# Optimization experiments

Measured on AMD Instinct MI355X. Metric: run time of the kernel, lower is better.

## Reference

```python
import jax, jax.numpy as jnp
import numpy as np

NUM_HEADS = 16
HEIGHT = 32
WIDTH = 32
FEATURES_DIM = HEIGHT * WIDTH  # 1024
EMBED_DIM = 1024


def setup_inputs() -> dict:
    key = jax.random.key(0)
    ks = jax.random.split(key, 9)
    s_in = 1.0 / np.sqrt(FEATURES_DIM)
    s_e = 1.0 / np.sqrt(EMBED_DIM)
    return {
        "x": jax.random.normal(ks[0], (16, 512, HEIGHT, WIDTH), dtype=jnp.float32),
        "Wq": jax.random.uniform(ks[1], (EMBED_DIM, FEATURES_DIM), jnp.float32, -s_in, s_in),
        "bq": jax.random.uniform(ks[2], (EMBED_DIM,), jnp.float32, -s_in, s_in),
        "Wk": jax.random.uniform(ks[3], (EMBED_DIM, FEATURES_DIM), jnp.float32, -s_in, s_in),
        "bk": jax.random.uniform(ks[4], (EMBED_DIM,), jnp.float32, -s_in, s_in),
        "Wv": jax.random.uniform(ks[5], (EMBED_DIM, FEATURES_DIM), jnp.float32, -s_in, s_in),
        "bv": jax.random.uniform(ks[6], (EMBED_DIM,), jnp.float32, -s_in, s_in),
        "Wo": jax.random.uniform(ks[7], (FEATURES_DIM, EMBED_DIM), jnp.float32, -s_e, s_e),
        "bo": jax.random.uniform(ks[8], (FEATURES_DIM,), jnp.float32, -s_e, s_e),
    }


def reference(x, Wq, bq, Wk, bk, Wv, bv, Wo, bo):
    B, C, H, W = x.shape
    nh = NUM_HEADS
    hd = EMBED_DIM // nh
    xf = x.reshape(B, C, H * W)  # [B, C, F] - channel tokens
    q = xf @ Wq.T + bq  # [B, C, E]
    k = xf @ Wk.T + bk
    v = xf @ Wv.T + bv
    q = q.reshape(B, C, nh, hd).transpose(0, 2, 1, 3)  # [B, nh, C, hd]
    k = k.reshape(B, C, nh, hd).transpose(0, 2, 1, 3)
    v = v.reshape(B, C, nh, hd).transpose(0, 2, 1, 3)
    scores = jnp.einsum("bhcd,bhkd->bhck", q, k) / jnp.sqrt(jnp.float32(hd))
    attn = jax.nn.softmax(scores, axis=-1)
    out = jnp.einsum("bhck,bhkd->bhcd", attn, v)  # [B, nh, C, hd]
    out = out.transpose(0, 2, 1, 3).reshape(B, C, EMBED_DIM)
    out = out @ Wo.T + bo  # [B, C, F]
    return out.reshape(B, C, H, W)
```

## Files before the change

### kernel.cpp

```cpp
#include <hip/hip_runtime.h>


typedef unsigned short u16;
typedef __attribute__((ext_vector_type(8))) short short8;
typedef __attribute__((ext_vector_type(4))) float f32x4;
typedef __attribute__((ext_vector_type(4))) unsigned short u16x4;

#define MFMA16(a, b, c) __builtin_amdgcn_mfma_f32_16x16x32_bf16(a, b, c, 0, 0, 0)

__device__ __forceinline__ u16 f2bf(float x) {
  unsigned u = __float_as_uint(x);
  u += 0x7FFFu + ((u >> 16) & 1u);
  return (u16)(u >> 16);
}

__device__ __forceinline__ void async16(const void* g, void* l) {
  __builtin_amdgcn_global_load_lds(
      (__attribute__((address_space(1))) unsigned int*)(g),
      (__attribute__((address_space(3))) unsigned int*)(l), 16, 0, 0);
}

__global__ __launch_bounds__(256) void cvt_all(
    const float* __restrict__ x, const float* __restrict__ wq,
    const float* __restrict__ wk, const float* __restrict__ wv,
    const float* __restrict__ wo, u16* __restrict__ dst) {
  int g = blockIdx.x * 256 + threadIdx.x;
  const float* s;
  int off;
  if (g < 2097152) {
    s = x; off = g;
  } else {
    int r = g - 2097152;
    int w = r >> 18;
    off = r & 262143;
    s = (w == 0) ? wq : (w == 1) ? wk : (w == 2) ? wv : wo;
  }
  f32x4 v = ((const f32x4*)s)[off];
  u16x4 o;
#pragma unroll
  for (int j = 0; j < 4; ++j) o[j] = f2bf(v[j]);
  ((u16x4*)dst)[g] = o;
}

__device__ __forceinline__ void gemm16(const u16* __restrict__ A,
                                       const u16* __restrict__ W,
                                       int m0, int n0, u16* lds,
                                       f32x4 acc[4][4]) {
  const int t = threadIdx.x;
  const int wave = t >> 6, lane = t & 63, lr = lane & 15, lg = lane >> 4;
  const int wr = wave >> 2, wn = wave & 3;
  const int srow = t >> 3;
  const int scol = ((t & 7) ^ ((t >> 3) & 7)) << 3;
  const u16* gA = A + (size_t)(m0 + srow) * 1024 + scol;
  const u16* gB = W + (size_t)(n0 + srow) * 1024 + scol;
  u16* stA = lds + wave * 512;
  u16* stB = lds + 8192 + wave * 512;
  const int aoff = (wr * 64 + lr) * 64;
  const int boff = 8192 + (wn * 64 + lr) * 64;
  const int sw0 = (lg ^ (lr & 7)) << 3;
  const int sw1 = ((4 ^ lg) ^ (lr & 7)) << 3;

#define STAGEA(buf, k0)                                     \
  {                                                         \
    async16(gA + (k0), stA + (buf) * 24576);                \
    async16(gA + 65536 + (k0), stA + (buf) * 24576 + 4096); \
  }
#define STAGEB1(buf, k0) async16(gB + (k0), stB + (buf) * 24576);
#define STAGEB3(buf, k0)                                       \
  {                                                            \
    async16(gB + 65536 + (k0), stB + (buf) * 24576 + 4096);    \
    async16(gB + 131072 + (k0), stB + (buf) * 24576 + 8192);   \
    async16(gB + 196608 + (k0), stB + (buf) * 24576 + 12288);  \
  }

  STAGEA(0, 0); STAGEB1(0, 0); STAGEB3(0, 0);
  STAGEA(1, 64); STAGEB1(1, 64); STAGEB3(1, 64);
  asm volatile("s_waitcnt vmcnt(6)" ::: "memory");
  __builtin_amdgcn_s_barrier();

#pragma unroll
  for (int tt = 0; tt < 16; ++tt) {
    const u16* bufp = lds + (tt % 3) * 24576;
    const int nb = (tt + 2) % 3, kn = (tt + 2) * 64;
    short8 av[4], bv[4];
#pragma unroll
    for (int m = 0; m < 4; ++m)
      av[m] = *(const short8*)(bufp + aoff + m * 1024 + sw0);
#pragma unroll
    for (int n = 0; n < 4; ++n)
      bv[n] = *(const short8*)(bufp + boff + n * 1024 + sw0);
    if (tt < 14) { STAGEA(nb, kn); STAGEB1(nb, kn); }
    __builtin_amdgcn_s_barrier();
    asm volatile("s_waitcnt lgkmcnt(0)" ::: "memory");
    __builtin_amdgcn_sched_barrier(0);
    __builtin_amdgcn_s_setprio(1);
#pragma unroll
    for (int m = 0; m < 4; ++m)
#pragma unroll
      for (int n = 0; n < 4; ++n)
        acc[m][n] = MFMA16(av[m], bv[n], acc[m][n]);
    __builtin_amdgcn_s_setprio(0);
    __builtin_amdgcn_s_barrier();
#pragma unroll
    for (int m = 0; m < 4; ++m)
      av[m] = *(const short8*)(bufp + aoff + m * 1024 + sw1);
#pragma unroll
    for (int n = 0; n < 4; ++n)
      bv[n] = *(const short8*)(bufp + boff + n * 1024 + sw1);
    if (tt < 14) STAGEB3(nb, kn);
    __builtin_amdgcn_s_barrier();
    asm volatile("s_waitcnt lgkmcnt(0)" ::: "memory");
    __builtin_amdgcn_sched_barrier(0);
    __builtin_amdgcn_s_setprio(1);
#pragma unroll
    for (int m = 0; m < 4; ++m)
#pragma unroll
      for (int n = 0; n < 4; ++n)
        acc[m][n] = MFMA16(av[m], bv[n], acc[m][n]);
    __builtin_amdgcn_s_setprio(0);
    if (tt < 14) {
      asm volatile("s_waitcnt vmcnt(6)" ::: "memory");
    } else {
      asm volatile("s_waitcnt vmcnt(0)" ::: "memory");
    }
    __builtin_amdgcn_s_barrier();
  }
#undef STAGEA
#undef STAGEB1
#undef STAGEB3
}

__global__ __launch_bounds__(512, 2) void gemm_qkv(
    const u16* __restrict__ xb, const u16* __restrict__ wq,
    const u16* __restrict__ wk, const u16* __restrict__ wv,
    const float* __restrict__ bq, const float* __restrict__ bk,
    const float* __restrict__ bv, u16* __restrict__ qo, u16* __restrict__ ko,
    u16* __restrict__ vo) {
  __shared__ u16 lds[73728];
  const int id = blockIdx.x;
  const int lid = (id & 7) * 96 + (id >> 3);
  const int z = lid >> 8;
  const int rem = lid & 255;
  const int m0 = (rem >> 2) * 128, n0 = (rem & 3) * 256;
  const u16* W = (z == 0) ? wq : (z == 1) ? wk : wv;
  const float* bias = (z == 0) ? bq : (z == 1) ? bk : bv;
  u16* outp = (z == 0) ? qo : (z == 1) ? ko : vo;
  f32x4 acc[4][4];
#pragma unroll
  for (int i = 0; i < 4; ++i)
#pragma unroll
    for (int j = 0; j < 4; ++j) acc[i][j] = (f32x4){0.f, 0.f, 0.f, 0.f};
  gemm16(xb, W, m0, n0, lds, acc);

  const int t = threadIdx.x;
  const int wave = t >> 6, lane = t & 63, lr = lane & 15, lg = lane >> 4;
  const int wr = wave >> 2, wn = wave & 3;
  float bb[4];
#pragma unroll
  for (int nf = 0; nf < 4; ++nf) bb[nf] = bias[n0 + wn * 64 + nf * 16 + lr];
#pragma unroll
  for (int mf = 0; mf < 4; ++mf)
#pragma unroll
    for (int nf = 0; nf < 4; ++nf)
#pragma unroll
      for (int r = 0; r < 4; ++r) {
        int m = m0 + wr * 64 + mf * 16 + lg * 4 + r;
        int n = n0 + wn * 64 + nf * 16 + lr;
        float val = acc[mf][nf][r] + bb[nf];
        int b_ = m >> 9, c = m & 511, h = n >> 6, dd = n & 63;
        int idx = (z == 2) ? ((((b_ << 4) + h) << 15) + (dd << 9) + c)
                           : ((((b_ << 4) + h) << 15) + (c << 6) + dd);
        outp[idx] = f2bf(val);
      }
}

__global__ __launch_bounds__(512, 2) void gemm_oproj(const u16* __restrict__ ab,
                                                     const u16* __restrict__ wo,
                                                     const float* __restrict__ bo,
                                                     float* __restrict__ out) {
  __shared__ u16 lds[73728];
  const int id = blockIdx.x;
  const int lid = (id & 7) * 32 + (id >> 3);
  const int m0 = (lid >> 2) * 128, n0 = (lid & 3) * 256;
  f32x4 acc[4][4];
#pragma unroll
  for (int i = 0; i < 4; ++i)
#pragma unroll
    for (int j = 0; j < 4; ++j) acc[i][j] = (f32x4){0.f, 0.f, 0.f, 0.f};
  gemm16(ab, wo, m0, n0, lds, acc);

  const int t = threadIdx.x;
  const int wave = t >> 6, lane = t & 63, lr = lane & 15, lg = lane >> 4;
  const int wr = wave >> 2, wn = wave & 3;
  float bb[4];
#pragma unroll
  for (int nf = 0; nf < 4; ++nf) bb[nf] = bo[n0 + wn * 64 + nf * 16 + lr];
#pragma unroll
  for (int mf = 0; mf < 4; ++mf)
#pragma unroll
    for (int nf = 0; nf < 4; ++nf)
#pragma unroll
      for (int r = 0; r < 4; ++r) {
        int m = m0 + wr * 64 + mf * 16 + lg * 4 + r;
        int n = n0 + wn * 64 + nf * 16 + lr;
        out[m * 1024 + n] = acc[mf][nf][r] + bb[nf];
      }
}

__global__ __launch_bounds__(512, 2) void attn_kernel(
    const u16* __restrict__ qb, const u16* __restrict__ kb,
    const u16* __restrict__ vb, u16* __restrict__ ab) {
  __shared__ u16 lK[32768];
  __shared__ u16 lV[32768];
  __shared__ u16 lP[8192];
  const int t = threadIdx.x;
  const int bh = blockIdx.x;
  const int b_ = bh >> 4, h_ = bh & 15;
  const u16* kg = kb + bh * 32768;
  const u16* vg = vb + bh * 32768;
#pragma unroll
  for (int i = 0; i < 8; ++i) {
    int row = i * 64 + (t >> 3), slot = t & 7;
    short8 kv = *(const short8*)(kg + row * 64 + slot * 8);
    *(short8*)(lK + row * 64 + ((slot ^ (row & 7)) << 3)) = kv;
    int vrow = i * 8 + (t >> 6), vslot = t & 63;
    short8 vv = *(const short8*)(vg + vrow * 512 + vslot * 8);
    *(short8*)(lV + vrow * 512 + ((vslot ^ (vrow & 7)) << 3)) = vv;
  }
  __syncthreads();

  const int wv_ = t >> 6, lane = t & 63, lr = lane & 15, lg = lane >> 4;
  u16* lPw = lP + wv_ * 1024;
  const u16* qg = qb + bh * 32768;
  const float sc = 0.125f * 1.44269504088896f;

#pragma unroll 1
  for (int qi = 0; qi < 4; ++qi) {
    const int qrow = (wv_ * 4 + qi) * 16;
    short8 a0 = *(const short8*)(qg + (qrow + lr) * 64 + lg * 8);
    short8 a1 = *(const short8*)(qg + (qrow + lr) * 64 + 32 + lg * 8);
    f32x4 s[32];
#pragma unroll
    for (int f = 0; f < 32; ++f) {
      const u16* kr = lK + (f * 16 + lr) * 64;
      short8 k0 = *(const short8*)(kr + ((lg ^ (lr & 7)) << 3));
      short8 k1 = *(const short8*)(kr + (((4 + lg) ^ (lr & 7)) << 3));
      f32x4 z4 = (f32x4){0.f, 0.f, 0.f, 0.f};
      z4 = MFMA16(a0, k0, z4);
      z4 = MFMA16(a1, k1, z4);
      s[f] = z4;
    }
    float inv[4];
#pragma unroll
    for (int r = 0; r < 4; ++r) {
      float m_ = s[0][r];
#pragma unroll
      for (int f = 1; f < 32; ++f) m_ = fmaxf(m_, s[f][r]);
      m_ = fmaxf(m_, __shfl_xor(m_, 1));
      m_ = fmaxf(m_, __shfl_xor(m_, 2));
      m_ = fmaxf(m_, __shfl_xor(m_, 4));
      m_ = fmaxf(m_, __shfl_xor(m_, 8));
      float sm = 0.f;
#pragma unroll
      for (int f = 0; f < 32; ++f) {
        float e = exp2f((s[f][r] - m_) * sc);
        s[f][r] = e;
        sm += e;
      }
      sm += __shfl_xor(sm, 1);
      sm += __shfl_xor(sm, 2);
      sm += __shfl_xor(sm, 4);
      sm += __shfl_xor(sm, 8);
      inv[r] = 1.f / sm;
    }
    f32x4 o[4];
#pragma unroll
    for (int i = 0; i < 4; ++i) o[i] = (f32x4){0.f, 0.f, 0.f, 0.f};
#pragma unroll
    for (int ch = 0; ch < 8; ++ch) {
#pragma unroll
      for (int cf = 0; cf < 4; ++cf)
#pragma unroll
        for (int r = 0; r < 4; ++r) {
          int q = lg * 4 + r, kc = cf * 16 + lr;
          lPw[q * 64 + (((kc >> 3) ^ (q & 7)) << 3) + (kc & 7)] =
              f2bf(s[ch * 4 + cf][r]);
        }
      asm volatile("s_waitcnt lgkmcnt(0)" ::: "memory");
      const u16* pr = lPw + lr * 64;
      short8 pa0 = *(const short8*)(pr + ((lg ^ (lr & 7)) << 3));
      short8 pa1 = *(const short8*)(pr + (((4 + lg) ^ (lr & 7)) << 3));
#pragma unroll
      for (int df = 0; df < 4; ++df) {
        const u16* vr = lV + (df * 16 + lr) * 512;
        short8 v0 = *(const short8*)(vr + (((ch * 8 + lg) ^ (lr & 7)) << 3));
        short8 v1 =
            *(const short8*)(vr + (((ch * 8 + 4 + lg) ^ (lr & 7)) << 3));
        o[df] = MFMA16(pa0, v0, o[df]);
        o[df] = MFMA16(pa1, v1, o[df]);
      }
    }
#pragma unroll
    for (int df = 0; df < 4; ++df)
#pragma unroll
      for (int r = 0; r < 4; ++r) {
        int q = qrow + lg * 4 + r, dd = df * 16 + lr;
        ab[(b_ * 512 + q) * 1024 + h_ * 64 + dd] = f2bf(o[df][r] * inv[r]);
      }
  }
}

extern "C" void kernel_launch(void* const* d_in, const int* in_sizes, int n_in,
                              void* d_out, int out_size, void* d_ws,
                              size_t ws_size, hipStream_t stream) {
  (void)in_sizes; (void)n_in; (void)out_size;
  const float* x  = (const float*)d_in[0];
  const float* Wq = (const float*)d_in[1];
  const float* bq = (const float*)d_in[2];
  const float* Wk = (const float*)d_in[3];
  const float* bk = (const float*)d_in[4];
  const float* Wv = (const float*)d_in[5];
  const float* bv = (const float*)d_in[6];
  const float* Wo = (const float*)d_in[7];
  const float* bo = (const float*)d_in[8];
  float* out = (float*)d_out;

  if (ws_size < 75497472u) return;
  u16* xb  = (u16*)d_ws;
  u16* wqb = xb + 8388608;
  u16* wkb = wqb + 1048576;
  u16* wvb = wkb + 1048576;
  u16* wob = wvb + 1048576;
  u16* qbuf = wob + 1048576;
  u16* kbuf = qbuf + 8388608;
  u16* vbuf = kbuf + 8388608;
  u16* abuf = xb;

  cvt_all<<<12288, 256, 0, stream>>>(x, Wq, Wk, Wv, Wo, xb);
  gemm_qkv<<<768, 512, 0, stream>>>(xb, wqb, wkb, wvb, bq, bk, bv,
                                    qbuf, kbuf, vbuf);
  attn_kernel<<<256, 512, 0, stream>>>(qbuf, kbuf, vbuf, abuf);
  gemm_oproj<<<256, 512, 0, stream>>>(abuf, wob, bo, out);
}
```

Before: 167.6 us.

## Enlarge GEMM tiles to 256x256 with double-buffered K pipeline

Both projection GEMMs now use 256x256 output tiles per 512-thread block, with each wave holding an 8x4 set of 16x16 accumulators. The K loop moves from a 3-stage ring of 64-wide slabs to a double-buffered scheme whose four MFMA quadrants are interleaved with the async global-to-LDS loads. The QKV weights are treated as one contiguous 3072-row matrix, so a block's N tile can span Q/K/V. This halves the grid sizes to raise arithmetic intensity and cut redundant A/B loads, at the cost of more accumulator registers and fewer blocks to fill the CUs.

```diff
diff --git a/kernel.cpp b/kernel.cpp
--- a/kernel.cpp
+++ b/kernel.cpp
@@ -42,115 +42,159 @@
   ((u16x4*)dst)[g] = o;
 }
 
-__device__ __forceinline__ void gemm16(const u16* __restrict__ A,
-                                       const u16* __restrict__ W,
-                                       int m0, int n0, u16* lds,
-                                       f32x4 acc[4][4]) {
+template <int CB, bool ST>
+__device__ __forceinline__ void tile256(const u16* lds, const u16* gA,
+                                        const u16* gB, u16* stA, u16* stB,
+                                        int kn, int arow, int brow, int sw0,
+                                        int sw1, short8* a, short8* b,
+                                        f32x4 acc[8][4]) {
+  constexpr int NB = CB ^ 1;
+  const u16* bp = lds + CB * 32768;
+#pragma unroll
+  for (int mf = 0; mf < 4; ++mf) {
+    a[mf * 2 + 0] = *(const short8*)(bp + arow + mf * 1024 + sw0);
+    a[mf * 2 + 1] = *(const short8*)(bp + arow + mf * 1024 + sw1);
+  }
+#pragma unroll
+  for (int nf = 0; nf < 2; ++nf) {
+    b[nf * 2 + 0] = *(const short8*)(bp + brow + nf * 1024 + sw0);
+    b[nf * 2 + 1] = *(const short8*)(bp + brow + nf * 1024 + sw1);
+  }
+  if (ST) {
+    async16(gA + 0 * 65536 + kn, stA + NB * 32768 + 0 * 4096);
+    async16(gA + 2 * 65536 + kn, stA + NB * 32768 + 2 * 4096);
+    async16(gB + 0 * 65536 + kn, stB + NB * 32768 + 0 * 4096);
+    async16(gB + 1 * 65536 + kn, stB + NB * 32768 + 1 * 4096);
+  }
+  __builtin_amdgcn_s_barrier();
+  asm volatile("s_waitcnt lgkmcnt(0)" ::: "memory");
+  __builtin_amdgcn_sched_barrier(0);
+  __builtin_amdgcn_s_setprio(1);
+#pragma unroll
+  for (int mf = 0; mf < 4; ++mf)
+#pragma unroll
+    for (int nf = 0; nf < 2; ++nf) {
+      acc[mf][nf] = MFMA16(a[mf * 2 + 0], b[nf * 2 + 0], acc[mf][nf]);
+      acc[mf][nf] = MFMA16(a[mf * 2 + 1], b[nf * 2 + 1], acc[mf][nf]);
+    }
+  __builtin_amdgcn_s_setprio(0);
+  __builtin_amdgcn_s_barrier();
+#pragma unroll
+  for (int nf = 2; nf < 4; ++nf) {
+    b[nf * 2 + 0] = *(const short8*)(bp + brow + nf * 1024 + sw0);
+    b[nf * 2 + 1] = *(const short8*)(bp + brow + nf * 1024 + sw1);
+  }
+  if (ST) {
+    async16(gB + 2 * 65536 + kn, stB + NB * 32768 + 2 * 4096);
+    async16(gB + 3 * 65536 + kn, stB + NB * 32768 + 3 * 4096);
+  }
+  __builtin_amdgcn_s_barrier();
+  asm volatile("s_waitcnt lgkmcnt(0)" ::: "memory");
+  __builtin_amdgcn_sched_barrier(0);
+  __builtin_amdgcn_s_setprio(1);
+#pragma unroll
+  for (int mf = 0; mf < 4; ++mf)
+#pragma unroll
+    for (int nf = 2; nf < 4; ++nf) {
+      acc[mf][nf] = MFMA16(a[mf * 2 + 0], b[nf * 2 + 0], acc[mf][nf]);
+      acc[mf][nf] = MFMA16(a[mf * 2 + 1], b[nf * 2 + 1], acc[mf][nf]);
+    }
+  __builtin_amdgcn_s_setprio(0);
+  __builtin_amdgcn_s_barrier();
+#pragma unroll
+  for (int mf = 4; mf < 8; ++mf) {
+    a[(mf - 4) * 2 + 0] = *(const short8*)(bp + arow + mf * 1024 + sw0);
+    a[(mf - 4) * 2 + 1] = *(const short8*)(bp + arow + mf * 1024 + sw1);
+  }
+  if (ST) {
+    async16(gA + 1 * 65536 + kn, stA + NB * 32768 + 1 * 4096);
+    async16(gA + 3 * 65536 + kn, stA + NB * 32768 + 3 * 4096);
+  }
+  __builtin_amdgcn_s_barrier();
+  asm volatile("s_waitcnt lgkmcnt(0)" ::: "memory");
+  __builtin_amdgcn_sched_barrier(0);
+  __builtin_amdgcn_s_setprio(1);
+#pragma unroll
+  for (int mf = 4; mf < 8; ++mf)
+#pragma unroll
+    for (int nf = 2; nf < 4; ++nf) {
+      acc[mf][nf] = MFMA16(a[(mf - 4) * 2 + 0], b[nf * 2 + 0], acc[mf][nf]);
+      acc[mf][nf] = MFMA16(a[(mf - 4) * 2 + 1], b[nf * 2 + 1], acc[mf][nf]);
+    }
+  __builtin_amdgcn_s_setprio(0);
+  __builtin_amdgcn_s_barrier();
+  __builtin_amdgcn_s_setprio(1);
+#pragma unroll
+  for (int mf = 4; mf < 8; ++mf)
+#pragma unroll
+    for (int nf = 0; nf < 2; ++nf) {
+      acc[mf][nf] = MFMA16(a[(mf - 4) * 2 + 0], b[nf * 2 + 0], acc[mf][nf]);
+      acc[mf][nf] = MFMA16(a[(mf - 4) * 2 + 1], b[nf * 2 + 1], acc[mf][nf]);
+    }
+  __builtin_amdgcn_s_setprio(0);
+  asm volatile("s_waitcnt vmcnt(0)" ::: "memory");
+  __builtin_amdgcn_s_barrier();
+}
+
+__device__ __forceinline__ void gemm256(const u16* __restrict__ A,
+                                        const u16* __restrict__ W, int m0,
+                                        int n0, u16* lds, f32x4 acc[8][4]) {
   const int t = threadIdx.x;
   const int wave = t >> 6, lane = t & 63, lr = lane & 15, lg = lane >> 4;
   const int wr = wave >> 2, wn = wave & 3;
   const int srow = t >> 3;
-  const int scol = ((t & 7) ^ ((t >> 3) & 7)) << 3;
+  const int scol = ((t & 7) ^ (srow & 7)) << 3;
   const u16* gA = A + (size_t)(m0 + srow) * 1024 + scol;
   const u16* gB = W + (size_t)(n0 + srow) * 1024 + scol;
   u16* stA = lds + wave * 512;
-  u16* stB = lds + 8192 + wave * 512;
-  const int aoff = (wr * 64 + lr) * 64;
-  const int boff = 8192 + (wn * 64 + lr) * 64;
-  const int sw0 = (lg ^ (lr & 7)) << 3;
-  const int sw1 = ((4 ^ lg) ^ (lr & 7)) << 3;
-
-#define STAGEA(buf, k0)                                     \
-  {                                                         \
-    async16(gA + (k0), stA + (buf) * 24576);                \
-    async16(gA + 65536 + (k0), stA + (buf) * 24576 + 4096); \
-  }
-#define STAGEB1(buf, k0) async16(gB + (k0), stB + (buf) * 24576);
-#define STAGEB3(buf, k0)                                       \
-  {                                                            \
-    async16(gB + 65536 + (k0), stB + (buf) * 24576 + 4096);    \
-    async16(gB + 131072 + (k0), stB + (buf) * 24576 + 8192);   \
-    async16(gB + 196608 + (k0), stB + (buf) * 24576 + 12288);  \
-  }
-
-  STAGEA(0, 0); STAGEB1(0, 0); STAGEB3(0, 0);
-  STAGEA(1, 64); STAGEB1(1, 64); STAGEB3(1, 64);
-  asm volatile("s_waitcnt vmcnt(6)" ::: "memory");
-  __builtin_amdgcn_s_barrier();
-
-#pragma unroll
-  for (int tt = 0; tt < 16; ++tt) {
-    const u16* bufp = lds + (tt % 3) * 24576;
-    const int nb = (tt + 2) % 3, kn = (tt + 2) * 64;
-    short8 av[4], bv[4];
-#pragma unroll
-    for (int m = 0; m < 4; ++m)
-      av[m] = *(const short8*)(bufp + aoff + m * 1024 + sw0);
-#pragma unroll
-    for (int n = 0; n < 4; ++n)
-      bv[n] = *(const short8*)(bufp + boff + n * 1024 + sw0);
-    if (tt < 14) { STAGEA(nb, kn); STAGEB1(nb, kn); }
-    __builtin_amdgcn_s_barrier();
-    asm volatile("s_waitcnt lgkmcnt(0)" ::: "memory");
-    __builtin_amdgcn_sched_barrier(0);
-    __builtin_amdgcn_s_setprio(1);
-#pragma unroll
-    for (int m = 0; m < 4; ++m)
-#pragma unroll
-      for (int n = 0; n < 4; ++n)
-        acc[m][n] = MFMA16(av[m], bv[n], acc[m][n]);
-    __builtin_amdgcn_s_setprio(0);
-    __builtin_amdgcn_s_barrier();
-#pragma unroll
-    for (int m = 0; m < 4; ++m)
-      av[m] = *(const short8*)(bufp + aoff + m * 1024 + sw1);
-#pragma unroll
-    for (int n = 0; n < 4; ++n)
-      bv[n] = *(const short8*)(bufp + boff + n * 1024 + sw1);
-    if (tt < 14) STAGEB3(nb, kn);
-    __builtin_amdgcn_s_barrier();
-    asm volatile("s_waitcnt lgkmcnt(0)" ::: "memory");
-    __builtin_amdgcn_sched_barrier(0);
-    __builtin_amdgcn_s_setprio(1);
-#pragma unroll
-    for (int m = 0; m < 4; ++m)
-#pragma unroll
-      for (int n = 0; n < 4; ++n)
-        acc[m][n] = MFMA16(av[m], bv[n], acc[m][n]);
-    __builtin_amdgcn_s_setprio(0);
-    if (tt < 14) {
-      asm volatile("s_waitcnt vmcnt(6)" ::: "memory");
-    } else {
-      asm volatile("s_waitcnt vmcnt(0)" ::: "memory");
-    }
-    __builtin_amdgcn_s_barrier();
-  }
-#undef STAGEA
-#undef STAGEB1
-#undef STAGEB3
+  u16* stB = lds + 16384 + wave * 512;
+  const int arow = (wr * 128 + lr) * 64;
+  const int brow = 16384 + (wn * 64 + lr) * 64;
+  const int xk = lr & 7;
+  const int sw0 = (lg ^ xk) << 3;
+  const int sw1 = ((4 + lg) ^ xk) << 3;
+
+#pragma unroll
+  for (int j = 0; j < 4; ++j) {
+    async16(gA + j * 65536, stA + j * 4096);
+    async16(gB + j * 65536, stB + j * 4096);
+  }
+  asm volatile("s_waitcnt vmcnt(0)" ::: "memory");
+  __builtin_amdgcn_s_barrier();
+
+  short8 a[8], b[8];
+#pragma unroll 1
+  for (int it = 0; it < 7; ++it) {
+    const int kt = it * 2;
+    tile256<0, true>(lds, gA, gB, stA, stB, (kt + 1) * 64, arow, brow, sw0,
+                     sw1, a, b, acc);
+    tile256<1, true>(lds, gA, gB, stA, stB, (kt + 2) * 64, arow, brow, sw0,
+                     sw1, a, b, acc);
+  }
+  tile256<0, true>(lds, gA, gB, stA, stB, 15 * 64, arow, brow, sw0, sw1, a, b,
+                   acc);
+  tile256<1, false>(lds, gA, gB, stA, stB, 0, arow, brow, sw0, sw1, a, b, acc);
 }
 
 __global__ __launch_bounds__(512, 2) void gemm_qkv(
-    const u16* __restrict__ xb, const u16* __restrict__ wq,
-    const u16* __restrict__ wk, const u16* __restrict__ wv,
+    const u16* __restrict__ xb, const u16* __restrict__ w3,
     const float* __restrict__ bq, const float* __restrict__ bk,
     const float* __restrict__ bv, u16* __restrict__ qo, u16* __restrict__ ko,
     u16* __restrict__ vo) {
-  __shared__ u16 lds[73728];
+  __shared__ u16 lds[65536];
   const int id = blockIdx.x;
-  const int lid = (id & 7) * 96 + (id >> 3);
-  const int z = lid >> 8;
-  const int rem = lid & 255;
-  const int m0 = (rem >> 2) * 128, n0 = (rem & 3) * 256;
-  const u16* W = (z == 0) ? wq : (z == 1) ? wk : wv;
+  const int lid = (id & 7) * 48 + (id >> 3);
+  const int tm = lid / 12, tn = lid % 12;
+  const int m0 = tm * 256, n0g = tn * 256;
+  const int z = n0g >> 10, n0 = n0g & 1023;
   const float* bias = (z == 0) ? bq : (z == 1) ? bk : bv;
   u16* outp = (z == 0) ? qo : (z == 1) ? ko : vo;
-  f32x4 acc[4][4];
-#pragma unroll
-  for (int i = 0; i < 4; ++i)
+  f32x4 acc[8][4];
+#pragma unroll
+  for (int i = 0; i < 8; ++i)
 #pragma unroll
     for (int j = 0; j < 4; ++j) acc[i][j] = (f32x4){0.f, 0.f, 0.f, 0.f};
-  gemm16(xb, W, m0, n0, lds, acc);
+  gemm256(xb, w3, m0, n0g, lds, acc);
 
   const int t = threadIdx.x;
   const int wave = t >> 6, lane = t & 63, lr = lane & 15, lg = lane >> 4;
@@ -159,12 +203,12 @@
 #pragma unroll
   for (int nf = 0; nf < 4; ++nf) bb[nf] = bias[n0 + wn * 64 + nf * 16 + lr];
 #pragma unroll
-  for (int mf = 0; mf < 4; ++mf)
+  for (int mf = 0; mf < 8; ++mf)
 #pragma unroll
     for (int nf = 0; nf < 4; ++nf)
 #pragma unroll
       for (int r = 0; r < 4; ++r) {
-        int m = m0 + wr * 64 + mf * 16 + lg * 4 + r;
+        int m = m0 + wr * 128 + mf * 16 + lg * 4 + r;
         int n = n0 + wn * 64 + nf * 16 + lr;
         float val = acc[mf][nf][r] + bb[nf];
         int b_ = m >> 9, c = m & 511, h = n >> 6, dd = n & 63;
@@ -178,16 +222,16 @@
                                                      const u16* __restrict__ wo,
                                                      const float* __restrict__ bo,
                                                      float* __restrict__ out) {
-  __shared__ u16 lds[73728];
+  __shared__ u16 lds[65536];
   const int id = blockIdx.x;
-  const int lid = (id & 7) * 32 + (id >> 3);
-  const int m0 = (lid >> 2) * 128, n0 = (lid & 3) * 256;
-  f32x4 acc[4][4];
-#pragma unroll
-  for (int i = 0; i < 4; ++i)
+  const int lid = (id & 7) * 16 + (id >> 3);
+  const int m0 = (lid >> 2) * 256, n0 = (lid & 3) * 256;
+  f32x4 acc[8][4];
+#pragma unroll
+  for (int i = 0; i < 8; ++i)
 #pragma unroll
     for (int j = 0; j < 4; ++j) acc[i][j] = (f32x4){0.f, 0.f, 0.f, 0.f};
-  gemm16(ab, wo, m0, n0, lds, acc);
+  gemm256(ab, wo, m0, n0, lds, acc);
 
   const int t = threadIdx.x;
   const int wave = t >> 6, lane = t & 63, lr = lane & 15, lg = lane >> 4;
@@ -196,12 +240,12 @@
 #pragma unroll
   for (int nf = 0; nf < 4; ++nf) bb[nf] = bo[n0 + wn * 64 + nf * 16 + lr];
 #pragma unroll
-  for (int mf = 0; mf < 4; ++mf)
+  for (int mf = 0; mf < 8; ++mf)
 #pragma unroll
     for (int nf = 0; nf < 4; ++nf)
 #pragma unroll
       for (int r = 0; r < 4; ++r) {
-        int m = m0 + wr * 64 + mf * 16 + lg * 4 + r;
+        int m = m0 + wr * 128 + mf * 16 + lg * 4 + r;
         int n = n0 + wn * 64 + nf * 16 + lr;
         out[m * 1024 + n] = acc[mf][nf][r] + bb[nf];
       }
@@ -327,18 +371,15 @@
 
   if (ws_size < 75497472u) return;
   u16* xb  = (u16*)d_ws;
-  u16* wqb = xb + 8388608;
-  u16* wkb = wqb + 1048576;
-  u16* wvb = wkb + 1048576;
-  u16* wob = wvb + 1048576;
+  u16* w3b = xb + 8388608;
+  u16* wob = w3b + 3145728;
   u16* qbuf = wob + 1048576;
   u16* kbuf = qbuf + 8388608;
   u16* vbuf = kbuf + 8388608;
   u16* abuf = xb;
 
   cvt_all<<<12288, 256, 0, stream>>>(x, Wq, Wk, Wv, Wo, xb);
-  gemm_qkv<<<768, 512, 0, stream>>>(xb, wqb, wkb, wvb, bq, bk, bv,
-                                    qbuf, kbuf, vbuf);
+  gemm_qkv<<<384, 512, 0, stream>>>(xb, w3b, bq, bk, bv, qbuf, kbuf, vbuf);
   attn_kernel<<<256, 512, 0, stream>>>(qbuf, kbuf, vbuf, abuf);
-  gemm_oproj<<<256, 512, 0, stream>>>(abuf, wob, bo, out);
-}
+  gemm_oproj<<<128, 512, 0, stream>>>(abuf, wob, bo, out);
+}
```

Measured after the change: 173.4 us. 3.5% more time.

## Replace 128x256 triple-buffered GEMM tile with 128x128 double-buffered K32 tile

Applied to the files above, without the earlier changes.

The shared GEMM core moves from a 128x256 tile with BK=64, triple buffering and 8 waves to a 128x128 tile with BK=32, double buffering and 4 waves. LDS per block drops from 144KB to 32KB, allowing three blocks per CU and doubling the grid of both projection GEMMs for better load balance. The QKV weights are addressed as one concatenated 3072-row matrix, and the tile index selects the q/k/v output. The cost is a simpler pipeline that waits on vmcnt(0) every iteration, weaker operand reuse per tile, and more global traffic.

```diff
diff --git a/kernel.cpp b/kernel.cpp
--- a/kernel.cpp
+++ b/kernel.cpp
@@ -42,107 +42,74 @@
   ((u16x4*)dst)[g] = o;
 }
 
-__device__ __forceinline__ void gemm16(const u16* __restrict__ A,
-                                       const u16* __restrict__ W,
-                                       int m0, int n0, u16* lds,
-                                       f32x4 acc[4][4]) {
+__device__ __forceinline__ void gemm128(const u16* __restrict__ A,
+                                        const u16* __restrict__ W, int m0,
+                                        int n0, u16* lds, f32x4 acc[4][4]) {
   const int t = threadIdx.x;
   const int wave = t >> 6, lane = t & 63, lr = lane & 15, lg = lane >> 4;
-  const int wr = wave >> 2, wn = wave & 3;
-  const int srow = t >> 3;
-  const int scol = ((t & 7) ^ ((t >> 3) & 7)) << 3;
+  const int wr = wave >> 1, wn = wave & 1;
+  const int srow = t >> 2;
+  const int scol = ((t & 3) ^ ((srow >> 1) & 3)) << 3;
   const u16* gA = A + (size_t)(m0 + srow) * 1024 + scol;
   const u16* gB = W + (size_t)(n0 + srow) * 1024 + scol;
   u16* stA = lds + wave * 512;
-  u16* stB = lds + 8192 + wave * 512;
-  const int aoff = (wr * 64 + lr) * 64;
-  const int boff = 8192 + (wn * 64 + lr) * 64;
-  const int sw0 = (lg ^ (lr & 7)) << 3;
-  const int sw1 = ((4 ^ lg) ^ (lr & 7)) << 3;
-
-#define STAGEA(buf, k0)                                     \
-  {                                                         \
-    async16(gA + (k0), stA + (buf) * 24576);                \
-    async16(gA + 65536 + (k0), stA + (buf) * 24576 + 4096); \
-  }
-#define STAGEB1(buf, k0) async16(gB + (k0), stB + (buf) * 24576);
-#define STAGEB3(buf, k0)                                       \
-  {                                                            \
-    async16(gB + 65536 + (k0), stB + (buf) * 24576 + 4096);    \
-    async16(gB + 131072 + (k0), stB + (buf) * 24576 + 8192);   \
-    async16(gB + 196608 + (k0), stB + (buf) * 24576 + 12288);  \
-  }
-
-  STAGEA(0, 0); STAGEB1(0, 0); STAGEB3(0, 0);
-  STAGEA(1, 64); STAGEB1(1, 64); STAGEB3(1, 64);
-  asm volatile("s_waitcnt vmcnt(6)" ::: "memory");
+  u16* stB = lds + 4096 + wave * 512;
+  const int arow = (wr * 64 + lr) * 32;
+  const int brow = 4096 + (wn * 64 + lr) * 32;
+  const int sw = (lg ^ ((lr >> 1) & 3)) << 3;
+
+#define STAGE(buf, k0)                                   \
+  {                                                      \
+    async16(gA + (k0), stA + (buf) * 8192);              \
+    async16(gA + 65536 + (k0), stA + (buf) * 8192 + 2048); \
+    async16(gB + (k0), stB + (buf) * 8192);              \
+    async16(gB + 65536 + (k0), stB + (buf) * 8192 + 2048); \
+  }
+
+  STAGE(0, 0);
+  asm volatile("s_waitcnt vmcnt(0)" ::: "memory");
   __builtin_amdgcn_s_barrier();
 
-#pragma unroll
-  for (int tt = 0; tt < 16; ++tt) {
-    const u16* bufp = lds + (tt % 3) * 24576;
-    const int nb = (tt + 2) % 3, kn = (tt + 2) * 64;
+#pragma unroll 2
+  for (int kt = 0; kt < 32; ++kt) {
+    const u16* bufp = lds + (kt & 1) * 8192;
+    if (kt < 31) {
+      const int nb = (kt + 1) & 1;
+      STAGE(nb, (kt + 1) * 32);
+    }
     short8 av[4], bv[4];
 #pragma unroll
-    for (int m = 0; m < 4; ++m)
-      av[m] = *(const short8*)(bufp + aoff + m * 1024 + sw0);
-#pragma unroll
-    for (int n = 0; n < 4; ++n)
-      bv[n] = *(const short8*)(bufp + boff + n * 1024 + sw0);
-    if (tt < 14) { STAGEA(nb, kn); STAGEB1(nb, kn); }
-    __builtin_amdgcn_s_barrier();
+    for (int mf = 0; mf < 4; ++mf)
+      av[mf] = *(const short8*)(bufp + arow + mf * 512 + sw);
+#pragma unroll
+    for (int nf = 0; nf < 4; ++nf)
+      bv[nf] = *(const short8*)(bufp + brow + nf * 512 + sw);
     asm volatile("s_waitcnt lgkmcnt(0)" ::: "memory");
     __builtin_amdgcn_sched_barrier(0);
     __builtin_amdgcn_s_setprio(1);
 #pragma unroll
-    for (int m = 0; m < 4; ++m)
-#pragma unroll
-      for (int n = 0; n < 4; ++n)
-        acc[m][n] = MFMA16(av[m], bv[n], acc[m][n]);
+    for (int mf = 0; mf < 4; ++mf)
+#pragma unroll
+      for (int nf = 0; nf < 4; ++nf)
+        acc[mf][nf] = MFMA16(av[mf], bv[nf], acc[mf][nf]);
     __builtin_amdgcn_s_setprio(0);
+    asm volatile("s_waitcnt vmcnt(0)" ::: "memory");
     __builtin_amdgcn_s_barrier();
-#pragma unroll
-    for (int m = 0; m < 4; ++m)
-      av[m] = *(const short8*)(bufp + aoff + m * 1024 + sw1);
-#pragma unroll
-    for (int n = 0; n < 4; ++n)
-      bv[n] = *(const short8*)(bufp + boff + n * 1024 + sw1);
-    if (tt < 14) STAGEB3(nb, kn);
-    __builtin_amdgcn_s_barrier();
-    asm volatile("s_waitcnt lgkmcnt(0)" ::: "memory");
-    __builtin_amdgcn_sched_barrier(0);
-    __builtin_amdgcn_s_setprio(1);
-#pragma unroll
-    for (int m = 0; m < 4; ++m)
-#pragma unroll
-      for (int n = 0; n < 4; ++n)
-        acc[m][n] = MFMA16(av[m], bv[n], acc[m][n]);
-    __builtin_amdgcn_s_setprio(0);
-    if (tt < 14) {
-      asm volatile("s_waitcnt vmcnt(6)" ::: "memory");
-    } else {
-      asm volatile("s_waitcnt vmcnt(0)" ::: "memory");
-    }
-    __builtin_amdgcn_s_barrier();
-  }
-#undef STAGEA
-#undef STAGEB1
-#undef STAGEB3
-}
-
-__global__ __launch_bounds__(512, 2) void gemm_qkv(
-    const u16* __restrict__ xb, const u16* __restrict__ wq,
-    const u16* __restrict__ wk, const u16* __restrict__ wv,
+  }
+#undef STAGE
+}
+
+__global__ __launch_bounds__(256, 3) void gemm_qkv(
+    const u16* __restrict__ xb, const u16* __restrict__ w3,
     const float* __restrict__ bq, const float* __restrict__ bk,
     const float* __restrict__ bv, u16* __restrict__ qo, u16* __restrict__ ko,
     u16* __restrict__ vo) {
-  __shared__ u16 lds[73728];
+  __shared__ u16 lds[16384];
   const int id = blockIdx.x;
-  const int lid = (id & 7) * 96 + (id >> 3);
-  const int z = lid >> 8;
-  const int rem = lid & 255;
-  const int m0 = (rem >> 2) * 128, n0 = (rem & 3) * 256;
-  const u16* W = (z == 0) ? wq : (z == 1) ? wk : wv;
+  const int lid = (id & 7) * 192 + (id >> 3);
+  const int tm = lid / 24, tn = lid % 24;
+  const int m0 = tm * 128, n0g = tn * 128;
+  const int z = n0g >> 10, n0 = n0g & 1023;
   const float* bias = (z == 0) ? bq : (z == 1) ? bk : bv;
   u16* outp = (z == 0) ? qo : (z == 1) ? ko : vo;
   f32x4 acc[4][4];
@@ -150,11 +117,11 @@
   for (int i = 0; i < 4; ++i)
 #pragma unroll
     for (int j = 0; j < 4; ++j) acc[i][j] = (f32x4){0.f, 0.f, 0.f, 0.f};
-  gemm16(xb, W, m0, n0, lds, acc);
+  gemm128(xb, w3, m0, n0g, lds, acc);
 
   const int t = threadIdx.x;
   const int wave = t >> 6, lane = t & 63, lr = lane & 15, lg = lane >> 4;
-  const int wr = wave >> 2, wn = wave & 3;
+  const int wr = wave >> 1, wn = wave & 1;
   float bb[4];
 #pragma unroll
   for (int nf = 0; nf < 4; ++nf) bb[nf] = bias[n0 + wn * 64 + nf * 16 + lr];
@@ -174,24 +141,23 @@
       }
 }
 
-__global__ __launch_bounds__(512, 2) void gemm_oproj(const u16* __restrict__ ab,
-                                                     const u16* __restrict__ wo,
-                                                     const float* __restrict__ bo,
-                                                     float* __restrict__ out) {
-  __shared__ u16 lds[73728];
+__global__ __launch_bounds__(256, 3) void gemm_oproj(
+    const u16* __restrict__ ab, const u16* __restrict__ wo,
+    const float* __restrict__ bo, float* __restrict__ out) {
+  __shared__ u16 lds[16384];
   const int id = blockIdx.x;
-  const int lid = (id & 7) * 32 + (id >> 3);
-  const int m0 = (lid >> 2) * 128, n0 = (lid & 3) * 256;
+  const int lid = (id & 7) * 64 + (id >> 3);
+  const int m0 = (lid >> 3) * 128, n0 = (lid & 7) * 128;
   f32x4 acc[4][4];
 #pragma unroll
   for (int i = 0; i < 4; ++i)
 #pragma unroll
     for (int j = 0; j < 4; ++j) acc[i][j] = (f32x4){0.f, 0.f, 0.f, 0.f};
-  gemm16(ab, wo, m0, n0, lds, acc);
+  gemm128(ab, wo, m0, n0, lds, acc);
 
   const int t = threadIdx.x;
   const int wave = t >> 6, lane = t & 63, lr = lane & 15, lg = lane >> 4;
-  const int wr = wave >> 2, wn = wave & 3;
+  const int wr = wave >> 1, wn = wave & 1;
   float bb[4];
 #pragma unroll
   for (int nf = 0; nf < 4; ++nf) bb[nf] = bo[n0 + wn * 64 + nf * 16 + lr];
@@ -327,18 +293,15 @@
 
   if (ws_size < 75497472u) return;
   u16* xb  = (u16*)d_ws;
-  u16* wqb = xb + 8388608;
-  u16* wkb = wqb + 1048576;
-  u16* wvb = wkb + 1048576;
-  u16* wob = wvb + 1048576;
+  u16* w3b = xb + 8388608;
+  u16* wob = w3b + 3145728;
   u16* qbuf = wob + 1048576;
   u16* kbuf = qbuf + 8388608;
   u16* vbuf = kbuf + 8388608;
   u16* abuf = xb;
 
   cvt_all<<<12288, 256, 0, stream>>>(x, Wq, Wk, Wv, Wo, xb);
-  gemm_qkv<<<768, 512, 0, stream>>>(xb, wqb, wkb, wvb, bq, bk, bv,
-                                    qbuf, kbuf, vbuf);
+  gemm_qkv<<<1536, 256, 0, stream>>>(xb, w3b, bq, bk, bv, qbuf, kbuf, vbuf);
   attn_kernel<<<256, 512, 0, stream>>>(qbuf, kbuf, vbuf, abuf);
-  gemm_oproj<<<256, 512, 0, stream>>>(abuf, wob, bo, out);
-}
+  gemm_oproj<<<512, 256, 0, stream>>>(abuf, wob, bo, out);
+}
```

After: 178.0 us. +6.2%, slower.
